# Optimization experiments

Measured on AMD Instinct MI355X. Metric: run time of the kernel, lower is better.

The kernel has to match this reference:

```python
import jax, jax.numpy as jnp
import numpy as np

H = 128  # hidden size
IN = 12  # input size
OUT = 4  # output classes


def _lstm_scan(gates_x, Whh, B, dtype, collect_ys):
    """gates_x: [T,B,4H] precomputed input-to-hidden gates (with biases).
    PyTorch gate order: i, f, g, o."""
    h0 = jnp.zeros((B, H), dtype)
    c0 = jnp.zeros((B, H), dtype)

    def step(carry, gx):
        h, c = carry
        g = gx + h @ Whh.T  # [B,4H]
        i, f, gg, o = jnp.split(g, 4, axis=-1)
        c = jax.nn.sigmoid(f) * c + jax.nn.sigmoid(i) * jnp.tanh(gg)
        h = jax.nn.sigmoid(o) * jnp.tanh(c)
        return (h, c), (h if collect_ys else None)

    (hT, cT), hs = jax.lax.scan(step, (h0, c0), gates_x)
    return hs, hT


def setup_inputs() -> dict:
    key = jax.random.key(0)
    ks = jax.random.split(key, 12)
    B, T = 256, 2048
    s = 1.0 / np.sqrt(H)  # torch LSTM/Linear init scale
    u = lambda k, shape: jax.random.uniform(k, shape, jnp.float32, -s, s)
    return {
        "x": jax.random.normal(ks[0], (B, T, IN), jnp.float32),
        "W_ih_l0": u(ks[1], (4 * H, IN)),
        "W_hh_l0": u(ks[2], (4 * H, H)),
        "b_ih_l0": u(ks[3], (4 * H,)),
        "b_hh_l0": u(ks[4], (4 * H,)),
        "W_ih_l1": u(ks[5], (4 * H, H)),
        "W_hh_l1": u(ks[6], (4 * H, H)),
        "b_ih_l1": u(ks[7], (4 * H,)),
        "b_hh_l1": u(ks[8], (4 * H,)),
        "W_out": u(ks[9], (OUT, H)),
        "b_out": u(ks[10], (OUT,)),
    }


def reference(x, W_ih_l0, W_hh_l0, b_ih_l0, b_hh_l0,
              W_ih_l1, W_hh_l1, b_ih_l1, b_hh_l1, W_out, b_out):
    B = x.shape[0]
    # layer 0: precompute all input projections at once -> [T,B,4H]
    gx0 = jnp.einsum('bti,gi->tbg', x, W_ih_l0) + b_ih_l0 + b_hh_l0
    hs0, _ = _lstm_scan(gx0, W_hh_l0, B, x.dtype, collect_ys=True)  # [T,B,H]
    # layer 1: only final hidden state is needed (r_out[:, -1] == h_T)
    gx1 = jnp.einsum('tbh,gh->tbg', hs0, W_ih_l1) + b_ih_l1 + b_hh_l1
    _, hT = _lstm_scan(gx1, W_hh_l1, B, x.dtype, collect_ys=False)  # [B,H]
    return hT @ W_out.T + b_out  # [B,4]
```

## Files before the change

### kernel.cpp

```cpp
#include <hip/hip_runtime.h>
#include <cstdint>
#include <cstddef>

#define H      128
#define IN_    12
#define GATES  512
#define B_     256
#define T_     2048
#define TCMAX  512
#define TI     32
#define PS     520

#define REP32(M) M(0) M(1) M(2) M(3) M(4) M(5) M(6) M(7) M(8) M(9) M(10) M(11) \
  M(12) M(13) M(14) M(15) M(16) M(17) M(18) M(19) M(20) M(21) M(22) M(23) \
  M(24) M(25) M(26) M(27) M(28) M(29) M(30) M(31)

__device__ __forceinline__ float sigmoidf_(float x) {
    return 1.f / (1.f + __expf(-x));
}
__device__ __forceinline__ float tanhf_(float x) {
    return 2.f / (1.f + __expf(-2.f * x)) - 1.f;
}
__device__ __forceinline__ float dot4f(float4 w, float4 h, float a) {
    return fmaf(w.x, h.x, fmaf(w.y, h.y, fmaf(w.z, h.z, fmaf(w.w, h.w, a))));
}

template<bool IS_L0>
__global__ __launch_bounds__(1024) void lstm_scan(
    const float* __restrict__ x_or_gx,
    const float* __restrict__ Wih,
    const float* __restrict__ Whh,
    const float* __restrict__ bih, const float* __restrict__ bhh,
    float* __restrict__ hs0,
    float* __restrict__ state,
    int tc, int chunk)
{
    const int b   = blockIdx.x;
    const int tid = threadIdx.x;
    const int ks  = tid >> 7;
    const int q   = tid & 127;

    extern __shared__ float smem[];
    float* sh_part = smem;
    float* sh_h    = smem + 8 * PS;
    float* sh_x    = sh_h + H;

#define LOADW(i) \
    const float4* wr##i = (const float4*)(Whh + (size_t)(4*q+i)*H + 16*ks); \
    float4 w##i##0 = wr##i[0], w##i##1 = wr##i[1], w##i##2 = wr##i[2], w##i##3 = wr##i[3];
    LOADW(0) LOADW(1) LOADW(2) LOADW(3)
#undef LOADW

    float4 wx0 = {0,0,0,0}, wx1 = {0,0,0,0}, wx2 = {0,0,0,0}, wx3 = {0,0,0,0};
    if constexpr (IS_L0) {
        if (ks >= 1 && ks <= 3) {
            wx0 = *(const float4*)(Wih + (size_t)(4*q+0)*IN_ + 4*(ks-1));
            wx1 = *(const float4*)(Wih + (size_t)(4*q+1)*IN_ + 4*(ks-1));
            wx2 = *(const float4*)(Wih + (size_t)(4*q+2)*IN_ + 4*(ks-1));
            wx3 = *(const float4*)(Wih + (size_t)(4*q+3)*IN_ + 4*(ks-1));
        }
        const float* xs = x_or_gx + ((size_t)b * T_ + (size_t)chunk * tc) * IN_;
        for (int i = tid; i < tc * IN_; i += 1024) sh_x[i] = xs[i];
    }

    float bias0 = 0, bias1 = 0, bias2 = 0, bias3 = 0;
    float cur0 = 0, cur1 = 0, cur2 = 0, cur3 = 0;
    float hreg = 0.f, creg = 0.f;
    const float* gxb = nullptr;
    if constexpr (!IS_L0) gxb = x_or_gx + (size_t)b * tc * GATES;

    if (tid < H) {
        if constexpr (IS_L0) {
            bias0 = bih[tid]         + bhh[tid];
            bias1 = bih[tid + 128]   + bhh[tid + 128];
            bias2 = bih[tid + 256]   + bhh[tid + 256];
            bias3 = bih[tid + 384]   + bhh[tid + 384];
        } else {
            cur0 = gxb[tid]; cur1 = gxb[tid + 128];
            cur2 = gxb[tid + 256]; cur3 = gxb[tid + 384];
        }
        if (chunk) { hreg = state[b*2*H + tid]; creg = state[b*2*H + H + tid]; }
        sh_h[tid] = hreg;
    }
    __syncthreads();

    float* hs_out = nullptr;
    if constexpr (IS_L0) hs_out = hs0 + (size_t)b * tc * H;

    const float4* sh4 = (const float4*)sh_h;
    const int i0 = tid & 3, q0 = tid >> 2;

    for (int t = 0; t < tc; ++t) {
        float n0 = 0, n1 = 0, n2 = 0, n3 = 0;
        if constexpr (!IS_L0) {
            if (tid < H) {
                int tn = (t + 1 < tc) ? t + 1 : t;
                const float* gp = gxb + (size_t)tn * GATES;
                n0 = gp[tid]; n1 = gp[tid + 128];
                n2 = gp[tid + 256]; n3 = gp[tid + 384];
            }
        }
        float4 hA = sh4[4*ks], hB = sh4[4*ks+1], hC = sh4[4*ks+2], hD = sh4[4*ks+3];
        float a0 = dot4f(w03,hD, dot4f(w02,hC, dot4f(w01,hB, dot4f(w00,hA, 0.f))));
        float a1 = dot4f(w13,hD, dot4f(w12,hC, dot4f(w11,hB, dot4f(w10,hA, 0.f))));
        float a2 = dot4f(w23,hD, dot4f(w22,hC, dot4f(w21,hB, dot4f(w20,hA, 0.f))));
        float a3 = dot4f(w33,hD, dot4f(w32,hC, dot4f(w31,hB, dot4f(w30,hA, 0.f))));
        if constexpr (IS_L0) {
            if (ks >= 1 && ks <= 3) {
                float4 xq = *(const float4*)(sh_x + t * IN_ + 4*(ks-1));
                a0 = dot4f(wx0, xq, a0); a1 = dot4f(wx1, xq, a1);
                a2 = dot4f(wx2, xq, a2); a3 = dot4f(wx3, xq, a3);
            }
        }
        sh_part[ks*PS + 0*128 + q] = a0;
        sh_part[ks*PS + 1*128 + q] = a1;
        sh_part[ks*PS + 2*128 + q] = a2;
        sh_part[ks*PS + 3*128 + q] = a3;
        __syncthreads();

        if (tid < H) {
            float p0, p1, p2, p3;
            {
                const float* pb = sh_part + i0*128 + q0;
#define RSUM(m, dst) { \
                float s = pb[32*m]; \
                s += pb[32*m + 1*PS]; s += pb[32*m + 2*PS]; s += pb[32*m + 3*PS]; \
                s += pb[32*m + 4*PS]; s += pb[32*m + 5*PS]; s += pb[32*m + 6*PS]; \
                s += pb[32*m + 7*PS]; dst = s; }
                RSUM(0, p0) RSUM(1, p1) RSUM(2, p2) RSUM(3, p3)
#undef RSUM
            }
            float gi, gf, gg, go;
            if constexpr (IS_L0) {
                gi = p0 + bias0; gf = p1 + bias1; gg = p2 + bias2; go = p3 + bias3;
            } else {
                gi = p0 + cur0; gf = p1 + cur1; gg = p2 + cur2; go = p3 + cur3;
                cur0 = n0; cur1 = n1; cur2 = n2; cur3 = n3;
            }
            creg = fmaf(sigmoidf_(gf), creg, sigmoidf_(gi) * tanhf_(gg));
            hreg = sigmoidf_(go) * tanhf_(creg);
            sh_h[tid] = hreg;
            if constexpr (IS_L0) hs_out[(size_t)t * H + tid] = hreg;
        }
        __syncthreads();
    }
    if (tid < H) { state[b*2*H + tid] = hreg; state[b*2*H + H + tid] = creg; }
}

__global__ __launch_bounds__(512) void gx1_gemm(
    const float* __restrict__ hs0, const float* __restrict__ Wih,
    const float* __restrict__ bih, const float* __restrict__ bhh,
    float* __restrict__ gx, int tc)
{
    const int b  = blockIdx.x;
    const int t0 = blockIdx.y * TI;
    const int g  = threadIdx.x;

    __shared__ alignas(16) float sh_h0[TI * H];

    const float4* src4 = (const float4*)(hs0 + ((size_t)b * tc + t0) * H);
    float4* dst4 = (float4*)sh_h0;
    for (int i = g; i < TI * H / 4; i += 512) dst4[i] = src4[i];

    const float biasg = bih[g] + bhh[g];
#define AI(t) float acc##t = biasg;
    REP32(AI)
#undef AI
    __syncthreads();

    const float4* wrow = (const float4*)(Wih + (size_t)g * H);
    const float4* sh4h = (const float4*)sh_h0;
    for (int k4 = 0; k4 < H / 4; ++k4) {
        float4 wq = wrow[k4];
#define PA(t) { float4 hv = sh4h[t*32 + k4]; \
        acc##t = fmaf(wq.x, hv.x, fmaf(wq.y, hv.y, fmaf(wq.z, hv.z, fmaf(wq.w, hv.w, acc##t)))); }
        REP32(PA)
#undef PA
    }

    float* gxo = gx + (size_t)b * tc * GATES;
#define SG(t) gxo[(size_t)(t0 + t) * GATES + g] = acc##t;
    REP32(SG)
#undef SG
}

__global__ void out_proj(const float* __restrict__ state1,
                         const float* __restrict__ Wout,
                         const float* __restrict__ bout,
                         float* __restrict__ out)
{
    const int b = blockIdx.x, j = threadIdx.x;
    __shared__ float sh[H];
    if (j < H) sh[j] = state1[b*2*H + j];
    __syncthreads();
    if (j < 4) {
        float a = bout[j];
        for (int k = 0; k < H; ++k) a = fmaf(Wout[j*H + k], sh[k], a);
        out[b*4 + j] = a;
    }
}

extern "C" void kernel_launch(void* const* d_in, const int* in_sizes, int n_in,
                              void* d_out, int out_size, void* d_ws, size_t ws_size,
                              hipStream_t stream)
{
    const float* x    = (const float*)d_in[0];
    const float* Wih0 = (const float*)d_in[1];
    const float* Whh0 = (const float*)d_in[2];
    const float* bih0 = (const float*)d_in[3];
    const float* bhh0 = (const float*)d_in[4];
    const float* Wih1 = (const float*)d_in[5];
    const float* Whh1 = (const float*)d_in[6];
    const float* bih1 = (const float*)d_in[7];
    const float* bhh1 = (const float*)d_in[8];
    const float* Wout = (const float*)d_in[9];
    const float* bout = (const float*)d_in[10];

    int tc = 32;
    for (int cand = TCMAX; cand >= 32; cand >>= 1) {
        size_t need = (size_t)2 * B_ * 2 * H * 4
                    + (size_t)B_ * cand * H * 4
                    + (size_t)B_ * cand * GATES * 4;
        if (need <= ws_size) { tc = cand; break; }
    }

    float* ws  = (float*)d_ws;
    float* st0 = ws;
    float* st1 = st0 + (size_t)B_ * 2 * H;
    float* hs0 = st1 + (size_t)B_ * 2 * H;
    float* gx1 = hs0 + (size_t)B_ * tc * H;

    const size_t shm_l0 = (size_t)(8 * PS + H + tc * IN_) * 4;
    const size_t shm_l1 = (size_t)(8 * PS + H) * 4;

    const int nchunks = T_ / tc;
    for (int c = 0; c < nchunks; ++c) {
        lstm_scan<true><<<B_, 1024, shm_l0, stream>>>(
            x, Wih0, Whh0, bih0, bhh0, hs0, st0, tc, c);
        gx1_gemm<<<dim3(B_, tc / TI), 512, 0, stream>>>(
            hs0, Wih1, bih1, bhh1, gx1, tc);
        lstm_scan<false><<<B_, 1024, shm_l1, stream>>>(
            gx1, nullptr, Whh1, nullptr, nullptr, nullptr, st1, tc, c);
    }
    out_proj<<<B_, 128, 0, stream>>>(st1, Wout, bout, (float*)d_out);
}
```

Baseline: 5.247 ms.

## Remap gate rows per thread for float4 partial reduction; register-resident W in gx1 GEMM

The recurrent scan now gives each thread the i/f/g/o gate rows for the same hidden unit q, so partial sums are written as one float4 and reduced with 8 vectorized LDS reads instead of 32 scalar strided reads. The per-step reduction in the serial critical path gets shorter. The gx1 GEMM now keeps each thread's W_ih row in 32 float4 registers and streams hs0 rows straight from global memory with broadcast loads, dropping the shared-memory staging and the 32 accumulators. The time tile grows to 64, with a waves-per-eu hint. This raises register pressure and relies on the cache for the hs0 broadcasts.

```diff
diff --git a/kernel.cpp b/kernel.cpp
--- a/kernel.cpp
+++ b/kernel.cpp
@@ -8,8 +8,7 @@
 #define B_     256
 #define T_     2048
 #define TCMAX  512
-#define TI     32
-#define PS     520
+#define TT     64
 
 #define REP32(M) M(0) M(1) M(2) M(3) M(4) M(5) M(6) M(7) M(8) M(9) M(10) M(11) \
   M(12) M(13) M(14) M(15) M(16) M(17) M(18) M(19) M(20) M(21) M(22) M(23) \
@@ -42,11 +41,11 @@
 
     extern __shared__ float smem[];
     float* sh_part = smem;
-    float* sh_h    = smem + 8 * PS;
+    float* sh_h    = smem + 8 * 512;
     float* sh_x    = sh_h + H;
 
 #define LOADW(i) \
-    const float4* wr##i = (const float4*)(Whh + (size_t)(4*q+i)*H + 16*ks); \
+    const float4* wr##i = (const float4*)(Whh + (size_t)(i * H + q) * H + 16 * ks); \
     float4 w##i##0 = wr##i[0], w##i##1 = wr##i[1], w##i##2 = wr##i[2], w##i##3 = wr##i[3];
     LOADW(0) LOADW(1) LOADW(2) LOADW(3)
 #undef LOADW
@@ -54,10 +53,10 @@
     float4 wx0 = {0,0,0,0}, wx1 = {0,0,0,0}, wx2 = {0,0,0,0}, wx3 = {0,0,0,0};
     if constexpr (IS_L0) {
         if (ks >= 1 && ks <= 3) {
-            wx0 = *(const float4*)(Wih + (size_t)(4*q+0)*IN_ + 4*(ks-1));
-            wx1 = *(const float4*)(Wih + (size_t)(4*q+1)*IN_ + 4*(ks-1));
-            wx2 = *(const float4*)(Wih + (size_t)(4*q+2)*IN_ + 4*(ks-1));
-            wx3 = *(const float4*)(Wih + (size_t)(4*q+3)*IN_ + 4*(ks-1));
+            wx0 = *(const float4*)(Wih + (size_t)(0 * H + q) * IN_ + 4 * (ks - 1));
+            wx1 = *(const float4*)(Wih + (size_t)(1 * H + q) * IN_ + 4 * (ks - 1));
+            wx2 = *(const float4*)(Wih + (size_t)(2 * H + q) * IN_ + 4 * (ks - 1));
+            wx3 = *(const float4*)(Wih + (size_t)(3 * H + q) * IN_ + 4 * (ks - 1));
         }
         const float* xs = x_or_gx + ((size_t)b * T_ + (size_t)chunk * tc) * IN_;
         for (int i = tid; i < tc * IN_; i += 1024) sh_x[i] = xs[i];
@@ -71,10 +70,10 @@
 
     if (tid < H) {
         if constexpr (IS_L0) {
-            bias0 = bih[tid]         + bhh[tid];
-            bias1 = bih[tid + 128]   + bhh[tid + 128];
-            bias2 = bih[tid + 256]   + bhh[tid + 256];
-            bias3 = bih[tid + 384]   + bhh[tid + 384];
+            bias0 = bih[tid]       + bhh[tid];
+            bias1 = bih[tid + 128] + bhh[tid + 128];
+            bias2 = bih[tid + 256] + bhh[tid + 256];
+            bias3 = bih[tid + 384] + bhh[tid + 384];
         } else {
             cur0 = gxb[tid]; cur1 = gxb[tid + 128];
             cur2 = gxb[tid + 256]; cur3 = gxb[tid + 384];
@@ -88,7 +87,8 @@
     if constexpr (IS_L0) hs_out = hs0 + (size_t)b * tc * H;
 
     const float4* sh4 = (const float4*)sh_h;
-    const int i0 = tid & 3, q0 = tid >> 2;
+    float4* sp4w = (float4*)sh_part;
+    const float4* sp4 = (const float4*)sh_part;
 
     for (int t = 0; t < tc; ++t) {
         float n0 = 0, n1 = 0, n2 = 0, n3 = 0;
@@ -107,34 +107,25 @@
         float a3 = dot4f(w33,hD, dot4f(w32,hC, dot4f(w31,hB, dot4f(w30,hA, 0.f))));
         if constexpr (IS_L0) {
             if (ks >= 1 && ks <= 3) {
-                float4 xq = *(const float4*)(sh_x + t * IN_ + 4*(ks-1));
+                float4 xq = *(const float4*)(sh_x + t * IN_ + 4 * (ks - 1));
                 a0 = dot4f(wx0, xq, a0); a1 = dot4f(wx1, xq, a1);
                 a2 = dot4f(wx2, xq, a2); a3 = dot4f(wx3, xq, a3);
             }
         }
-        sh_part[ks*PS + 0*128 + q] = a0;
-        sh_part[ks*PS + 1*128 + q] = a1;
-        sh_part[ks*PS + 2*128 + q] = a2;
-        sh_part[ks*PS + 3*128 + q] = a3;
+        float4 av; av.x = a0; av.y = a1; av.z = a2; av.w = a3;
+        sp4w[ks * 128 + q] = av;
         __syncthreads();
 
         if (tid < H) {
-            float p0, p1, p2, p3;
-            {
-                const float* pb = sh_part + i0*128 + q0;
-#define RSUM(m, dst) { \
-                float s = pb[32*m]; \
-                s += pb[32*m + 1*PS]; s += pb[32*m + 2*PS]; s += pb[32*m + 3*PS]; \
-                s += pb[32*m + 4*PS]; s += pb[32*m + 5*PS]; s += pb[32*m + 6*PS]; \
-                s += pb[32*m + 7*PS]; dst = s; }
-                RSUM(0, p0) RSUM(1, p1) RSUM(2, p2) RSUM(3, p3)
-#undef RSUM
-            }
+            float pi = 0, pf = 0, pg = 0, po = 0;
+#define RQ(m) { float4 v = sp4[m * 128 + tid]; pi += v.x; pf += v.y; pg += v.z; po += v.w; }
+            RQ(0) RQ(1) RQ(2) RQ(3) RQ(4) RQ(5) RQ(6) RQ(7)
+#undef RQ
             float gi, gf, gg, go;
             if constexpr (IS_L0) {
-                gi = p0 + bias0; gf = p1 + bias1; gg = p2 + bias2; go = p3 + bias3;
+                gi = pi + bias0; gf = pf + bias1; gg = pg + bias2; go = po + bias3;
             } else {
-                gi = p0 + cur0; gf = p1 + cur1; gg = p2 + cur2; go = p3 + cur3;
+                gi = pi + cur0; gf = pf + cur1; gg = pg + cur2; go = po + cur3;
                 cur0 = n0; cur1 = n1; cur2 = n2; cur3 = n3;
             }
             creg = fmaf(sigmoidf_(gf), creg, sigmoidf_(gi) * tanhf_(gg));
@@ -147,41 +138,35 @@
     if (tid < H) { state[b*2*H + tid] = hreg; state[b*2*H + H + tid] = creg; }
 }
 
-__global__ __launch_bounds__(512) void gx1_gemm(
-    const float* __restrict__ hs0, const float* __restrict__ Wih,
-    const float* __restrict__ bih, const float* __restrict__ bhh,
-    float* __restrict__ gx, int tc)
+__global__ __launch_bounds__(512)
+__attribute__((amdgpu_waves_per_eu(2, 2)))
+void gx1_gemm(const float* __restrict__ hs0, const float* __restrict__ Wih,
+              const float* __restrict__ bih, const float* __restrict__ bhh,
+              float* __restrict__ gx, int tc)
 {
     const int b  = blockIdx.x;
-    const int t0 = blockIdx.y * TI;
+    const int t0 = blockIdx.y * TT;
     const int g  = threadIdx.x;
 
-    __shared__ alignas(16) float sh_h0[TI * H];
-
-    const float4* src4 = (const float4*)(hs0 + ((size_t)b * tc + t0) * H);
-    float4* dst4 = (float4*)sh_h0;
-    for (int i = g; i < TI * H / 4; i += 512) dst4[i] = src4[i];
-
+#define LWG(j) float4 w##j = ((const float4*)(Wih + (size_t)g * H))[j];
+    REP32(LWG)
+#undef LWG
     const float biasg = bih[g] + bhh[g];
-#define AI(t) float acc##t = biasg;
-    REP32(AI)
-#undef AI
-    __syncthreads();
-
-    const float4* wrow = (const float4*)(Wih + (size_t)g * H);
-    const float4* sh4h = (const float4*)sh_h0;
-    for (int k4 = 0; k4 < H / 4; ++k4) {
-        float4 wq = wrow[k4];
-#define PA(t) { float4 hv = sh4h[t*32 + k4]; \
-        acc##t = fmaf(wq.x, hv.x, fmaf(wq.y, hv.y, fmaf(wq.z, hv.z, fmaf(wq.w, hv.w, acc##t)))); }
-        REP32(PA)
-#undef PA
-    }
-
-    float* gxo = gx + (size_t)b * tc * GATES;
-#define SG(t) gxo[(size_t)(t0 + t) * GATES + g] = acc##t;
-    REP32(SG)
-#undef SG
+
+    const float* hp = hs0 + ((size_t)b * tc + t0) * H;
+    float* gxo = gx + ((size_t)b * tc + t0) * GATES + g;
+
+    for (int t = 0; t < TT; ++t) {
+        const float4* h4 = (const float4*)(hp + (size_t)t * H);
+        float a0 = biasg, a1 = 0.f, a2 = 0.f, a3 = 0.f;
+#define G4(i0,i1,i2,i3) \
+        a0 = dot4f(w##i0, h4[i0], a0); a1 = dot4f(w##i1, h4[i1], a1); \
+        a2 = dot4f(w##i2, h4[i2], a2); a3 = dot4f(w##i3, h4[i3], a3);
+        G4(0,1,2,3)    G4(4,5,6,7)    G4(8,9,10,11)   G4(12,13,14,15)
+        G4(16,17,18,19) G4(20,21,22,23) G4(24,25,26,27) G4(28,29,30,31)
+#undef G4
+        gxo[(size_t)t * GATES] = (a0 + a1) + (a2 + a3);
+    }
 }
 
 __global__ void out_proj(const float* __restrict__ state1,
@@ -216,8 +201,8 @@
     const float* Wout = (const float*)d_in[9];
     const float* bout = (const float*)d_in[10];
 
-    int tc = 32;
-    for (int cand = TCMAX; cand >= 32; cand >>= 1) {
+    int tc = TT;
+    for (int cand = TCMAX; cand >= TT; cand >>= 1) {
         size_t need = (size_t)2 * B_ * 2 * H * 4
                     + (size_t)B_ * cand * H * 4
                     + (size_t)B_ * cand * GATES * 4;
@@ -230,14 +215,14 @@
     float* hs0 = st1 + (size_t)B_ * 2 * H;
     float* gx1 = hs0 + (size_t)B_ * tc * H;
 
-    const size_t shm_l0 = (size_t)(8 * PS + H + tc * IN_) * 4;
-    const size_t shm_l1 = (size_t)(8 * PS + H) * 4;
+    const size_t shm_l0 = (size_t)(8 * 512 + H + tc * IN_) * 4;
+    const size_t shm_l1 = (size_t)(8 * 512 + H) * 4;
 
     const int nchunks = T_ / tc;
     for (int c = 0; c < nchunks; ++c) {
         lstm_scan<true><<<B_, 1024, shm_l0, stream>>>(
             x, Wih0, Whh0, bih0, bhh0, hs0, st0, tc, c);
-        gx1_gemm<<<dim3(B_, tc / TI), 512, 0, stream>>>(
+        gx1_gemm<<<dim3(B_, tc / TT), 512, 0, stream>>>(
             hs0, Wih1, bih1, bhh1, gx1, tc);
         lstm_scan<false><<<B_, 1024, shm_l1, stream>>>(
             gx1, nullptr, Whh1, nullptr, nullptr, nullptr, st1, tc, c);
```

Result: slower. 7.907 ms (median of 4 runs) (+50.7%).

## Rewrite gx1 GEMM with register-resident weights and scalar-loaded hidden states

Applied to the files above, without the earlier changes.

The layer-1 input-projection GEMM now holds each thread's full 128-element weight row in registers. Hidden-state rows are broadcast to the wave through inline-asm s_load_dwordx16 scalar loads, replacing the shared-memory staging and the block barrier. Each thread computes one gate output per timestep with four independent accumulators, and the time tile grows from 32 to 64. This removes LDS traffic and sync, but adds heavy VGPR use (128 weight floats), serialized scalar-load waits every half row, and a larger minimum chunk size.

```diff
diff --git a/kernel.cpp b/kernel.cpp
--- a/kernel.cpp
+++ b/kernel.cpp
@@ -8,7 +8,7 @@
 #define B_     256
 #define T_     2048
 #define TCMAX  512
-#define TI     32
+#define TT     64
 #define PS     520
 
 #define REP32(M) M(0) M(1) M(2) M(3) M(4) M(5) M(6) M(7) M(8) M(9) M(10) M(11) \
@@ -71,10 +71,10 @@
 
     if (tid < H) {
         if constexpr (IS_L0) {
-            bias0 = bih[tid]         + bhh[tid];
-            bias1 = bih[tid + 128]   + bhh[tid + 128];
-            bias2 = bih[tid + 256]   + bhh[tid + 256];
-            bias3 = bih[tid + 384]   + bhh[tid + 384];
+            bias0 = bih[tid]       + bhh[tid];
+            bias1 = bih[tid + 128] + bhh[tid + 128];
+            bias2 = bih[tid + 256] + bhh[tid + 256];
+            bias3 = bih[tid + 384] + bhh[tid + 384];
         } else {
             cur0 = gxb[tid]; cur1 = gxb[tid + 128];
             cur2 = gxb[tid + 256]; cur3 = gxb[tid + 384];
@@ -147,41 +147,68 @@
     if (tid < H) { state[b*2*H + tid] = hreg; state[b*2*H + H + tid] = creg; }
 }
 
-__global__ __launch_bounds__(512) void gx1_gemm(
-    const float* __restrict__ hs0, const float* __restrict__ Wih,
-    const float* __restrict__ bih, const float* __restrict__ bhh,
-    float* __restrict__ gx, int tc)
+typedef __attribute__((ext_vector_type(16))) float f16x;
+
+__global__ __launch_bounds__(512)
+void gx1_gemm(const float* __restrict__ hs0, const float* __restrict__ Wih,
+              const float* __restrict__ bih, const float* __restrict__ bhh,
+              float* __restrict__ gx, int tc)
 {
     const int b  = blockIdx.x;
-    const int t0 = blockIdx.y * TI;
+    const int t0 = blockIdx.y * TT;
     const int g  = threadIdx.x;
 
-    __shared__ alignas(16) float sh_h0[TI * H];
-
-    const float4* src4 = (const float4*)(hs0 + ((size_t)b * tc + t0) * H);
-    float4* dst4 = (float4*)sh_h0;
-    for (int i = g; i < TI * H / 4; i += 512) dst4[i] = src4[i];
-
+#define LWG(j) float4 w##j = ((const float4*)(Wih + (size_t)g * H))[j];
+    REP32(LWG)
+#undef LWG
     const float biasg = bih[g] + bhh[g];
-#define AI(t) float acc##t = biasg;
-    REP32(AI)
-#undef AI
-    __syncthreads();
-
-    const float4* wrow = (const float4*)(Wih + (size_t)g * H);
-    const float4* sh4h = (const float4*)sh_h0;
-    for (int k4 = 0; k4 < H / 4; ++k4) {
-        float4 wq = wrow[k4];
-#define PA(t) { float4 hv = sh4h[t*32 + k4]; \
-        acc##t = fmaf(wq.x, hv.x, fmaf(wq.y, hv.y, fmaf(wq.z, hv.z, fmaf(wq.w, hv.w, acc##t)))); }
-        REP32(PA)
-#undef PA
-    }
-
-    float* gxo = gx + (size_t)b * tc * GATES;
-#define SG(t) gxo[(size_t)(t0 + t) * GATES + g] = acc##t;
-    REP32(SG)
-#undef SG
+
+    const float* hp = hs0 + ((size_t)b * tc + t0) * H;
+    float* gxo = gx + ((size_t)b * tc + t0) * GATES + g;
+
+    for (int t = 0; t < TT; ++t) {
+        const float* hpt = hp + (size_t)t * H;
+        float a0 = biasg, a1 = 0.f, a2 = 0.f, a3 = 0.f;
+
+        f16x h0, h1, h2, h3;
+        asm volatile(
+            "s_load_dwordx16 %0, %4, 0x0\n\t"
+            "s_load_dwordx16 %1, %4, 0x40\n\t"
+            "s_load_dwordx16 %2, %4, 0x80\n\t"
+            "s_load_dwordx16 %3, %4, 0xc0\n\t"
+            "s_waitcnt lgkmcnt(0)"
+            : "=s"(h0), "=s"(h1), "=s"(h2), "=s"(h3)
+            : "s"(hpt));
+#define FMA16(hv, base) { \
+        a0 = fmaf(w##base.x, hv.s0, a0);  a1 = fmaf(w##base.y, hv.s1, a1); \
+        a2 = fmaf(w##base.z, hv.s2, a2);  a3 = fmaf(w##base.w, hv.s3, a3); }
+#define Q4(hv, j0, j1, j2, j3) { \
+        a0 = fmaf(w##j0.x, hv.s0, a0); a1 = fmaf(w##j0.y, hv.s1, a1); \
+        a2 = fmaf(w##j0.z, hv.s2, a2); a3 = fmaf(w##j0.w, hv.s3, a3); \
+        a0 = fmaf(w##j1.x, hv.s4, a0); a1 = fmaf(w##j1.y, hv.s5, a1); \
+        a2 = fmaf(w##j1.z, hv.s6, a2); a3 = fmaf(w##j1.w, hv.s7, a3); \
+        a0 = fmaf(w##j2.x, hv.s8, a0); a1 = fmaf(w##j2.y, hv.s9, a1); \
+        a2 = fmaf(w##j2.z, hv.sa, a2); a3 = fmaf(w##j2.w, hv.sb, a3); \
+        a0 = fmaf(w##j3.x, hv.sc, a0); a1 = fmaf(w##j3.y, hv.sd, a1); \
+        a2 = fmaf(w##j3.z, hv.se, a2); a3 = fmaf(w##j3.w, hv.sf, a3); }
+        Q4(h0, 0, 1, 2, 3)    Q4(h1, 4, 5, 6, 7)
+        Q4(h2, 8, 9, 10, 11)  Q4(h3, 12, 13, 14, 15)
+
+        asm volatile(
+            "s_load_dwordx16 %0, %4, 0x100\n\t"
+            "s_load_dwordx16 %1, %4, 0x140\n\t"
+            "s_load_dwordx16 %2, %4, 0x180\n\t"
+            "s_load_dwordx16 %3, %4, 0x1c0\n\t"
+            "s_waitcnt lgkmcnt(0)"
+            : "=s"(h0), "=s"(h1), "=s"(h2), "=s"(h3)
+            : "s"(hpt));
+        Q4(h0, 16, 17, 18, 19)  Q4(h1, 20, 21, 22, 23)
+        Q4(h2, 24, 25, 26, 27)  Q4(h3, 28, 29, 30, 31)
+#undef Q4
+#undef FMA16
+
+        gxo[(size_t)t * GATES] = (a0 + a1) + (a2 + a3);
+    }
 }
 
 __global__ void out_proj(const float* __restrict__ state1,
@@ -216,8 +243,8 @@
     const float* Wout = (const float*)d_in[9];
     const float* bout = (const float*)d_in[10];
 
-    int tc = 32;
-    for (int cand = TCMAX; cand >= 32; cand >>= 1) {
+    int tc = TT;
+    for (int cand = TCMAX; cand >= TT; cand >>= 1) {
         size_t need = (size_t)2 * B_ * 2 * H * 4
                     + (size_t)B_ * cand * H * 4
                     + (size_t)B_ * cand * GATES * 4;
@@ -237,7 +264,7 @@
     for (int c = 0; c < nchunks; ++c) {
         lstm_scan<true><<<B_, 1024, shm_l0, stream>>>(
             x, Wih0, Whh0, bih0, bhh0, hs0, st0, tc, c);
-        gx1_gemm<<<dim3(B_, tc / TI), 512, 0, stream>>>(
+        gx1_gemm<<<dim3(B_, tc / TT), 512, 0, stream>>>(
             hs0, Wih1, bih1, bhh1, gx1, tc);
         lstm_scan<false><<<B_, 1024, shm_l1, stream>>>(
             gx1, nullptr, Whh1, nullptr, nullptr, nullptr, st1, tc, c);
```

Result: slower. 5.653 ms (+7.7%).
